# Performance work log

Hardware: AMD Instinct MI355X
Metric: run time of the kernel (lower is better)

Reference implementation:

```python
import jax, jax.numpy as jnp
import numpy as np

HEADS = 16


def setup_inputs() -> dict:
    key = jax.random.key(0)
    ks = jax.random.split(key, 5)
    n, s, d = 2, 2048, 1024
    return {
        "x": jax.random.normal(ks[0], (n, s, d), dtype=jnp.float32),
        "Wqkv": jax.random.normal(ks[1], (3 * d, d), dtype=jnp.float32) * (d ** -0.5),
        "bqkv": jax.random.normal(ks[2], (3 * d,), dtype=jnp.float32) * 0.02,
        "Wd": jax.random.normal(ks[3], (d, d), dtype=jnp.float32) * (d ** -0.5),
        "bd": jax.random.normal(ks[4], (d,), dtype=jnp.float32) * 0.02,
        "mask": 1,
    }


def reference(x, Wqkv, bqkv, Wd, bd, mask):
    n, s, d = x.shape
    h = HEADS
    hd = d // h
    qkv = x @ Wqkv.T + bqkv  # [n, s, 3d]
    q, k, v = jnp.split(qkv, 3, axis=-1)
    # [n, h, s, hd]
    q = q.reshape(n, s, h, hd).transpose(0, 2, 1, 3)
    k = k.reshape(n, s, h, hd).transpose(0, 2, 1, 3)
    v = v.reshape(n, s, h, hd).transpose(0, 2, 1, 3)
    scores = jnp.einsum("bhqd,bhkd->bhqk", q, k)
    if mask:
        causal = jnp.triu(jnp.ones((s, s), dtype=bool), k=1)
        scores = jnp.where(causal, -jnp.inf, scores)
    attn = jax.nn.softmax(scores / jnp.sqrt(jnp.float32(hd)), axis=-1)
    out = jnp.einsum("bhqk,bhkd->bhqd", attn, v)
    out = out.transpose(0, 2, 1, 3).reshape(n, s, d)
    return out @ Wd.T + bd
```

## Files before the change

### kernel.cpp

```cpp
#include <hip/hip_runtime.h>
#include <hip/hip_bf16.h>
#include <cstdint>
#include <cstddef>

typedef __attribute__((ext_vector_type(8))) short bf8_t;
typedef __attribute__((ext_vector_type(4))) float f4_t;

__device__ __forceinline__ unsigned short f2bf(float f) {
    union { float f; unsigned int u; } v; v.f = f;
    unsigned int u = v.u + 0x7FFFu + ((v.u >> 16) & 1u);
    return (unsigned short)(u >> 16);
}

__device__ __forceinline__ void gl_lds16(const void* g, void* l) {
    __builtin_amdgcn_global_load_lds(
        (const __attribute__((address_space(1))) unsigned int*)g,
        (__attribute__((address_space(3))) unsigned int*)l,
        16, 0, 0);
}

__global__ void cvt_kernel(const float* __restrict__ x,    unsigned short* __restrict__ xb,
                           const float* __restrict__ wq,   unsigned short* __restrict__ wqb,
                           const float* __restrict__ wd,   unsigned short* __restrict__ wdb) {
    int i = blockIdx.x * blockDim.x + threadIdx.x;
    const float* src; unsigned short* dst; int off;
    if (i < 1048576)       { src = x;  dst = xb;  off = i; }
    else if (i < 1835008)  { src = wq; dst = wqb; off = i - 1048576; }
    else                   { src = wd; dst = wdb; off = i - 1835008; }
    float4 f = ((const float4*)src)[off];
    ushort4 o;
    o.x = f2bf(f.x); o.y = f2bf(f.y); o.z = f2bf(f.z); o.w = f2bf(f.w);
    ((ushort4*)dst)[off] = o;
}

template<int MODE>
__global__ __launch_bounds__(256, 2) void gemm_bt_kernel(
    const unsigned short* __restrict__ A,
    const unsigned short* __restrict__ W,
    const float* __restrict__ bias,
    float* __restrict__ outf,
    unsigned short* __restrict__ qb,
    unsigned short* __restrict__ kb,
    unsigned short* __restrict__ vtb,
    int K, int Nn)
{
    __shared__ unsigned short As[64][32];
    __shared__ unsigned short Bs[128][32];

    const int tid  = threadIdx.x;
    const int lane = tid & 63;
    const int w    = tid >> 6;
    const int wm   = w & 1;
    const int wn   = w >> 1;
    const int quad = lane >> 4;
    const int l16  = lane & 15;
    const int m0   = blockIdx.y * 64;
    const int n0   = blockIdx.x * 128;

    const int lrow = lane >> 2;
    const int lcol = (lane & 3) << 3;

    f4_t acc[2][4];
    {
        f4_t z = {0.f, 0.f, 0.f, 0.f};
        #pragma unroll
        for (int i = 0; i < 2; ++i)
            #pragma unroll
            for (int j = 0; j < 4; ++j) acc[i][j] = z;
    }

    const unsigned short* Ag0 = A + (size_t)(m0 + w * 16 + lrow) * K + lcol;
    const unsigned short* Bg0 = W + (size_t)(n0 + w * 16 + lrow) * K + lcol;
    const unsigned short* Bg1 = W + (size_t)(n0 + 64 + w * 16 + lrow) * K + lcol;
    unsigned short* lA0 = &As[w * 16][0];
    unsigned short* lB0 = &Bs[w * 16][0];
    unsigned short* lB1 = &Bs[64 + w * 16][0];

    for (int kk = 0; kk < K; kk += 32) {
        __syncthreads();
        gl_lds16(Ag0 + kk, lA0);
        gl_lds16(Bg0 + kk, lB0);
        gl_lds16(Bg1 + kk, lB1);
        __syncthreads();

        bf8_t af[2], bfr[4];
        #pragma unroll
        for (int mb = 0; mb < 2; ++mb)
            af[mb] = *(const bf8_t*)&As[wm * 32 + mb * 16 + l16][quad * 8];
        #pragma unroll
        for (int nb = 0; nb < 4; ++nb)
            bfr[nb] = *(const bf8_t*)&Bs[wn * 64 + nb * 16 + l16][quad * 8];
        #pragma unroll
        for (int mb = 0; mb < 2; ++mb)
            #pragma unroll
            for (int nb = 0; nb < 4; ++nb)
                acc[mb][nb] = __builtin_amdgcn_mfma_f32_16x16x32_bf16(af[mb], bfr[nb], acc[mb][nb], 0, 0, 0);
    }

    #pragma unroll
    for (int nb = 0; nb < 4; ++nb) {
        const int col = n0 + wn * 64 + nb * 16 + l16;
        const float bc = bias[col];
        const int which  = col >> 10;
        const int within = col & 1023;
        const int head   = within >> 6;
        const int hdi    = within & 63;
        #pragma unroll
        for (int mb = 0; mb < 2; ++mb) {
            #pragma unroll
            for (int r = 0; r < 4; ++r) {
                const int row = m0 + wm * 32 + mb * 16 + quad * 4 + r;
                const float v = acc[mb][nb][r] + bc;
                if (MODE == 0) {
                    const int b  = row >> 11;
                    const int sq = row & 2047;
                    const int bh = b * 16 + head;
                    const unsigned short bv = f2bf(v);
                    if (which == 0)      qb [((size_t)bh * 2048 + sq) * 64 + hdi] = bv;
                    else if (which == 1) kb [((size_t)bh * 2048 + sq) * 64 + hdi] = bv;
                    else                 vtb[((size_t)bh * 64 + hdi) * 2048 + sq] = bv;
                } else {
                    outf[(size_t)row * Nn + col] = v;
                }
            }
        }
    }
}

__global__ __launch_bounds__(256, 2) void attn_kernel(
    const unsigned short* __restrict__ qg,
    const unsigned short* __restrict__ kg,
    const unsigned short* __restrict__ vg,
    unsigned short* __restrict__ ao)
{
    __shared__ unsigned short QP[64][72];
    __shared__ unsigned short Ks[2][64][72];
    __shared__ unsigned short Vs[2][64][72];

    const int tid  = threadIdx.x;
    const int lane = tid & 63;
    const int w    = tid >> 6;
    const int quad = lane >> 4;
    const int l16  = lane & 15;
    const int bx   = blockIdx.x;
    const int bh   = ((bx & 7) << 2) + ((bx >> 3) & 3);
    const int jj   = bx >> 5;
    const int qtBig   = 31 - jj;
    const int qtSmall = jj;
    const int b    = bh >> 4;
    const int head = bh & 15;

    const unsigned short* Qp = qg + (size_t)bh * 2048 * 64;
    const unsigned short* Kp = kg + (size_t)bh * 2048 * 64;
    const unsigned short* Vp = vg + (size_t)bh * 64 * 2048;

    const int sr = tid >> 2;
    const int sc = (tid & 3) << 4;

    float4 q0a = *(const float4*)(Qp + (size_t)(qtBig * 64 + sr) * 64 + sc);
    float4 q0b = *(const float4*)(Qp + (size_t)(qtBig * 64 + sr) * 64 + sc + 8);
    float4 q1a = *(const float4*)(Qp + (size_t)(qtSmall * 64 + sr) * 64 + sc);
    float4 q1b = *(const float4*)(Qp + (size_t)(qtSmall * 64 + sr) * 64 + sc + 8);

    float4 k0 = *(const float4*)(Kp + (size_t)sr * 64 + sc);
    float4 k1 = *(const float4*)(Kp + (size_t)sr * 64 + sc + 8);
    float4 v0 = *(const float4*)(Vp + (size_t)sr * 2048 + sc);
    float4 v1 = *(const float4*)(Vp + (size_t)sr * 2048 + sc + 8);

    *(float4*)&QP[sr][sc]     = q0a;
    *(float4*)&QP[sr][sc + 8] = q0b;
    bf8_t aq[2];
    aq[0] = *(const bf8_t*)&QP[w * 16 + l16][quad * 8];
    aq[1] = *(const bf8_t*)&QP[w * 16 + l16][32 + quad * 8];

    bf8_t bones;
    {
        const short one = (l16 == 0) ? (short)0x3F80 : (short)0;
        #pragma unroll
        for (int j = 0; j < 8; ++j) bones[j] = one;
    }

    f4_t oacc[4];
    f4_t lacc;
    {
        f4_t z = {0.f, 0.f, 0.f, 0.f};
        #pragma unroll
        for (int j = 0; j < 4; ++j) oacc[j] = z;
        lacc = z;
    }

    auto epilogue = [&](int qt) {
        #pragma unroll
        for (int r = 0; r < 4; ++r) {
            const float lsum = __shfl(lacc[r], lane & 48);
            const float rl = 1.f / lsum;
            const int sq = qt * 64 + (w << 4) + (quad << 2) + r;
            #pragma unroll
            for (int nb = 0; nb < 4; ++nb) {
                const int dcol = head * 64 + nb * 16 + l16;
                ao[((size_t)(b * 2048 + sq)) * 1024 + dcol] = f2bf(oacc[nb][r] * rl);
            }
        }
    };

    const int p0len = 32 - jj;

    for (int t = 0; t < 33; ++t) {
        const int buf = t & 1;
        *(float4*)&Ks[buf][sr][sc]     = k0;
        *(float4*)&Ks[buf][sr][sc + 8] = k1;
        *(float4*)&Vs[buf][sr][sc]     = v0;
        *(float4*)&Vs[buf][sr][sc + 8] = v1;
        __syncthreads();

        if (t + 1 < 33) {
            const int t2 = t + 1;
            const size_t sk = (size_t)((t2 >= p0len) ? (t2 - p0len) : t2) << 6;
            k0 = *(const float4*)(Kp + (sk + sr) * 64 + sc);
            k1 = *(const float4*)(Kp + (sk + sr) * 64 + sc + 8);
            v0 = *(const float4*)(Vp + (size_t)sr * 2048 + sk + sc);
            v1 = *(const float4*)(Vp + (size_t)sr * 2048 + sk + sc + 8);
        }

        if (t == p0len) {
            epilogue(qtBig);
            f4_t z = {0.f, 0.f, 0.f, 0.f};
            #pragma unroll
            for (int j = 0; j < 4; ++j) oacc[j] = z;
            lacc = z;
            *(float4*)&QP[sr][sc]     = q1a;
            *(float4*)&QP[sr][sc + 8] = q1b;
            aq[0] = *(const bf8_t*)&QP[w * 16 + l16][quad * 8];
            aq[1] = *(const bf8_t*)&QP[w * 16 + l16][32 + quad * 8];
        }

        const bool ph1 = (t >= p0len);
        const int  kt  = ph1 ? (t - p0len) : t;
        const int  qt  = ph1 ? qtSmall : qtBig;
        const bool diag = (kt == qt);

        f4_t sacc[4];
        {
            f4_t z = {0.f, 0.f, 0.f, 0.f};
            #pragma unroll
            for (int j = 0; j < 4; ++j) sacc[j] = z;
        }
        #pragma unroll
        for (int ks = 0; ks < 2; ++ks) {
            #pragma unroll
            for (int nb = 0; nb < 4; ++nb) {
                bf8_t bk = *(const bf8_t*)&Ks[buf][nb * 16 + l16][ks * 32 + quad * 8];
                sacc[nb] = __builtin_amdgcn_mfma_f32_16x16x32_bf16(aq[ks], bk, sacc[nb], 0, 0, 0);
            }
        }

        #pragma unroll
        for (int r = 0; r < 4; ++r) {
            const int rloc = (w << 4) + (quad << 2) + r;
            #pragma unroll
            for (int nb = 0; nb < 4; ++nb) {
                float e = fmaf(sacc[nb][r], 0.18033688f, -20.197731f);
                if (diag && (nb * 16 + l16 > rloc)) e = -1e30f;
                union { float f; unsigned int u; } pv;
                pv.f = exp2f(e);
                QP[rloc][nb * 16 + l16] = (unsigned short)(pv.u >> 16);
            }
        }

        #pragma unroll
        for (int ks = 0; ks < 2; ++ks) {
            bf8_t ap = *(const bf8_t*)&QP[(w << 4) + l16][ks * 32 + quad * 8];
            #pragma unroll
            for (int nb = 0; nb < 4; ++nb) {
                bf8_t bv = *(const bf8_t*)&Vs[buf][nb * 16 + l16][ks * 32 + quad * 8];
                oacc[nb] = __builtin_amdgcn_mfma_f32_16x16x32_bf16(ap, bv, oacc[nb], 0, 0, 0);
            }
            lacc = __builtin_amdgcn_mfma_f32_16x16x32_bf16(ap, bones, lacc, 0, 0, 0);
        }
    }

    epilogue(qtSmall);
}

extern "C" void kernel_launch(void* const* d_in, const int* in_sizes, int n_in,
                              void* d_out, int out_size, void* d_ws, size_t ws_size,
                              hipStream_t stream) {
    const float* x    = (const float*)d_in[0];
    const float* Wqkv = (const float*)d_in[1];
    const float* bqkv = (const float*)d_in[2];
    const float* Wd   = (const float*)d_in[3];
    const float* bd   = (const float*)d_in[4];
    float* out = (float*)d_out;

    char* ws = (char*)d_ws;
    unsigned short* xb    = (unsigned short*)(ws);
    unsigned short* wqkvb = (unsigned short*)(ws + 8388608);
    unsigned short* wdb   = (unsigned short*)(ws + 14680064);
    unsigned short* qb2   = (unsigned short*)(ws + 16777216);
    unsigned short* kb2   = (unsigned short*)(ws + 25165824);
    unsigned short* vtb   = (unsigned short*)(ws + 33554432);
    unsigned short* ao    = xb;

    cvt_kernel<<<8192, 256, 0, stream>>>(x, xb, Wqkv, wqkvb, Wd, wdb);

    gemm_bt_kernel<0><<<dim3(24, 64), 256, 0, stream>>>(
        xb, wqkvb, bqkv, nullptr, qb2, kb2, vtb, 1024, 3072);

    attn_kernel<<<512, 256, 0, stream>>>(qb2, kb2, vtb, ao);

    gemm_bt_kernel<1><<<dim3(8, 64), 256, 0, stream>>>(
        ao, wdb, bd, out, nullptr, nullptr, nullptr, 1024, 1024);
}
```

Measured before the change: 203.0 us.

## Widen GEMM K-tile to 64 with XOR-swizzled LDS and larger M tile

```diff
diff --git a/kernel.cpp b/kernel.cpp
--- a/kernel.cpp
+++ b/kernel.cpp
@@ -33,7 +33,7 @@
     ((ushort4*)dst)[off] = o;
 }
 
-template<int MODE>
+template<int MODE, int TM>
 __global__ __launch_bounds__(256, 2) void gemm_bt_kernel(
     const unsigned short* __restrict__ A,
     const unsigned short* __restrict__ W,
@@ -44,8 +44,12 @@
     unsigned short* __restrict__ vtb,
     int K, int Nn)
 {
-    __shared__ unsigned short As[64][32];
-    __shared__ unsigned short Bs[128][32];
+    constexpr int HM = TM / 2;
+    constexpr int MB = HM / 16;
+    constexpr int AI = TM / 32;
+
+    __shared__ unsigned short As[TM][64];
+    __shared__ unsigned short Bs[128][64];
 
     const int tid  = threadIdx.x;
     const int lane = tid & 63;
@@ -54,47 +58,52 @@
     const int wn   = w >> 1;
     const int quad = lane >> 4;
     const int l16  = lane & 15;
-    const int m0   = blockIdx.y * 64;
+    const int m0   = blockIdx.y * TM;
     const int n0   = blockIdx.x * 128;
 
-    const int lrow = lane >> 2;
-    const int lcol = (lane & 3) << 3;
-
-    f4_t acc[2][4];
+    const int lrow = lane >> 3;
+    const int lcol = ((lane & 7) ^ lrow) << 3;
+
+    f4_t acc[MB][4];
     {
         f4_t z = {0.f, 0.f, 0.f, 0.f};
         #pragma unroll
-        for (int i = 0; i < 2; ++i)
+        for (int i = 0; i < MB; ++i)
             #pragma unroll
             for (int j = 0; j < 4; ++j) acc[i][j] = z;
     }
 
-    const unsigned short* Ag0 = A + (size_t)(m0 + w * 16 + lrow) * K + lcol;
-    const unsigned short* Bg0 = W + (size_t)(n0 + w * 16 + lrow) * K + lcol;
-    const unsigned short* Bg1 = W + (size_t)(n0 + 64 + w * 16 + lrow) * K + lcol;
-    unsigned short* lA0 = &As[w * 16][0];
-    unsigned short* lB0 = &Bs[w * 16][0];
-    unsigned short* lB1 = &Bs[64 + w * 16][0];
-
-    for (int kk = 0; kk < K; kk += 32) {
+    const unsigned short* Agp = A + (size_t)(m0 + w * (TM / 4) + lrow) * K + lcol;
+    const unsigned short* Bgp = W + (size_t)(n0 + w * 32 + lrow) * K + lcol;
+    unsigned short* lAp = &As[w * (TM / 4)][0];
+    unsigned short* lBp = &Bs[w * 32][0];
+
+    for (int kk = 0; kk < K; kk += 64) {
         __syncthreads();
-        gl_lds16(Ag0 + kk, lA0);
-        gl_lds16(Bg0 + kk, lB0);
-        gl_lds16(Bg1 + kk, lB1);
+        #pragma unroll
+        for (int i = 0; i < AI; ++i)
+            gl_lds16(Agp + (size_t)(i * 8) * K + kk, lAp + i * 8 * 64);
+        #pragma unroll
+        for (int i = 0; i < 4; ++i)
+            gl_lds16(Bgp + (size_t)(i * 8) * K + kk, lBp + i * 8 * 64);
         __syncthreads();
 
-        bf8_t af[2], bfr[4];
-        #pragma unroll
-        for (int mb = 0; mb < 2; ++mb)
-            af[mb] = *(const bf8_t*)&As[wm * 32 + mb * 16 + l16][quad * 8];
-        #pragma unroll
-        for (int nb = 0; nb < 4; ++nb)
-            bfr[nb] = *(const bf8_t*)&Bs[wn * 64 + nb * 16 + l16][quad * 8];
-        #pragma unroll
-        for (int mb = 0; mb < 2; ++mb)
+        const int sw = l16 & 7;
+        #pragma unroll
+        for (int ks = 0; ks < 2; ++ks) {
+            bf8_t af[MB], bfr[4];
+            #pragma unroll
+            for (int mb = 0; mb < MB; ++mb)
+                af[mb] = *(const bf8_t*)&As[wm * HM + mb * 16 + l16][(((ks << 2) | quad) ^ sw) << 3];
             #pragma unroll
             for (int nb = 0; nb < 4; ++nb)
-                acc[mb][nb] = __builtin_amdgcn_mfma_f32_16x16x32_bf16(af[mb], bfr[nb], acc[mb][nb], 0, 0, 0);
+                bfr[nb] = *(const bf8_t*)&Bs[wn * 64 + nb * 16 + l16][(((ks << 2) | quad) ^ sw) << 3];
+            #pragma unroll
+            for (int mb = 0; mb < MB; ++mb)
+                #pragma unroll
+                for (int nb = 0; nb < 4; ++nb)
+                    acc[mb][nb] = __builtin_amdgcn_mfma_f32_16x16x32_bf16(af[mb], bfr[nb], acc[mb][nb], 0, 0, 0);
+        }
     }
 
     #pragma unroll
@@ -106,10 +115,10 @@
         const int head   = within >> 6;
         const int hdi    = within & 63;
         #pragma unroll
-        for (int mb = 0; mb < 2; ++mb) {
+        for (int mb = 0; mb < MB; ++mb) {
             #pragma unroll
             for (int r = 0; r < 4; ++r) {
-                const int row = m0 + wm * 32 + mb * 16 + quad * 4 + r;
+                const int row = m0 + wm * HM + mb * 16 + quad * 4 + r;
                 const float v = acc[mb][nb][r] + bc;
                 if (MODE == 0) {
                     const int b  = row >> 11;
@@ -303,11 +312,11 @@
 
     cvt_kernel<<<8192, 256, 0, stream>>>(x, xb, Wqkv, wqkvb, Wd, wdb);
 
-    gemm_bt_kernel<0><<<dim3(24, 64), 256, 0, stream>>>(
+    gemm_bt_kernel<0, 128><<<dim3(24, 32), 256, 0, stream>>>(
         xb, wqkvb, bqkv, nullptr, qb2, kb2, vtb, 1024, 3072);
 
     attn_kernel<<<512, 256, 0, stream>>>(qb2, kb2, vtb, ao);
 
-    gemm_bt_kernel<1><<<dim3(8, 64), 256, 0, stream>>>(
+    gemm_bt_kernel<1, 64><<<dim3(8, 64), 256, 0, stream>>>(
         ao, wdb, bd, out, nullptr, nullptr, nullptr, 1024, 1024);
 }
```

Result: faster. 183.4 us (-9.7%).
